# Kernel tuning notes

Hardware: AMD Instinct MI355X
Metric: run time of the kernel (lower is better)

The kernel has to match this reference:

```python
import jax, jax.numpy as jnp
import numpy as np

THRESHOLD = 1000.0  # `threshold` is undefined in the original source; fixed hyperparameter here.


def setup_inputs() -> dict:
    key = jax.random.key(0)
    k1, k2 = jax.random.split(key)
    N, C = 262144, 128
    output = jax.random.normal(k1, (N, C), dtype=jnp.float32)
    target = jax.random.randint(k2, (N,), 0, C, dtype=jnp.int64)
    return {"output": output, "target": target}


def reference(output, target):
    n, c = output.shape
    tgt = target.astype(jnp.int32)
    # score at the target class, per row
    tgt_scores = jnp.take_along_axis(output, tgt[:, None], axis=1)[:, 0]
    # max over the non-target classes (target entry masked to -inf)
    is_tgt = jnp.arange(c)[None, :] == tgt[:, None]
    others_max = jnp.max(jnp.where(is_tgt, -jnp.inf, output), axis=1)
    margin = tgt_scores - others_max
    # soft hinge loss per example
    fst = jax.nn.relu(1.0 - margin)
    snd = jax.nn.relu(1.0 - tgt_scores + jax.scipy.special.logsumexp(output, axis=1))
    l = jnp.where(margin >= 0, fst, snd)
    # partial_opt: sort, cumulative-sum threshold selection, scatter mask back
    order = jnp.argsort(l)
    sorted_l = l[order]
    cum = jnp.cumsum(sorted_l)
    sel = (cum <= THRESHOLD - jnp.arange(n, dtype=l.dtype)).astype(l.dtype)
    v = jnp.zeros((n,), l.dtype).at[order].set(sel)
    curriculum_loss_1 = jnp.dot(v, l)
    curriculum_loss_2 = jnp.asarray(n, l.dtype) - jnp.sum(v)
    return jnp.where(curriculum_loss_1 < curriculum_loss_2, curriculum_loss_2, curriculum_loss_1)
```

## Files before the change

### kernel.cpp

```cpp
#include <hip/hip_runtime.h>
#include <math.h>
#include <stdint.h>


static constexpr int   NBINS     = 128;
static constexpr int   GRID1     = 256;
static constexpr int   BLK1     = 1024;
static constexpr int   CNT_SHIFT = 44;
static constexpr unsigned long long SUM_MASK = (1ULL << CNT_SHIFT) - 1;
static constexpr float BIN_SCALE = 8.0f;
static constexpr float FIX_SCALE = 1048576.0f;
static constexpr double FIX_INV  = 1.0 / 1048576.0;

__device__ __forceinline__ float row_loss(float4 p0, float4 p1, int t, int lane)
{
    const int sl = lane & 15;
    const float v0 = p0.x, v1 = p0.y, v2 = p0.z, v3 = p0.w;
    const float v4 = p1.x, v5 = p1.y, v6 = p1.z, v7 = p1.w;
    const int c0 = sl * 4;
    const int c1 = 64 + sl * 4;

    float mall = fmaxf(fmaxf(fmaxf(v0, v1), fmaxf(v2, v3)),
                       fmaxf(fmaxf(v4, v5), fmaxf(v6, v7)));

    float e0 = (c0 + 0 == t) ? -INFINITY : v0;
    float e1 = (c0 + 1 == t) ? -INFINITY : v1;
    float e2 = (c0 + 2 == t) ? -INFINITY : v2;
    float e3 = (c0 + 3 == t) ? -INFINITY : v3;
    float e4 = (c1 + 0 == t) ? -INFINITY : v4;
    float e5 = (c1 + 1 == t) ? -INFINITY : v5;
    float e6 = (c1 + 2 == t) ? -INFINITY : v6;
    float e7 = (c1 + 3 == t) ? -INFINITY : v7;
    float mexc = fmaxf(fmaxf(fmaxf(e0, e1), fmaxf(e2, e3)),
                       fmaxf(fmaxf(e4, e5), fmaxf(e6, e7)));

    #pragma unroll
    for (int off = 8; off; off >>= 1) {
        mall = fmaxf(mall, __shfl_xor(mall, off));
        mexc = fmaxf(mexc, __shfl_xor(mexc, off));
    }

    float se = __expf(v0 - mall) + __expf(v1 - mall)
             + __expf(v2 - mall) + __expf(v3 - mall)
             + __expf(v4 - mall) + __expf(v5 - mall)
             + __expf(v6 - mall) + __expf(v7 - mall);
    #pragma unroll
    for (int off = 8; off; off >>= 1) se += __shfl_xor(se, off);

    const int te = t & 3;
    const float lo = (te == 0) ? v0 : (te == 1) ? v1 : (te == 2) ? v2 : v3;
    const float hi = (te == 0) ? v4 : (te == 1) ? v5 : (te == 2) ? v6 : v7;
    const float tsv = (t < 64) ? lo : hi;
    const float ts  = __shfl(tsv, (lane & 48) | ((t >> 2) & 15));

    const float margin = ts - mexc;
    const float lse    = mall + __logf(se);
    const float fst    = fmaxf(1.0f - margin, 0.0f);
    const float snd    = fmaxf(1.0f - ts + lse, 0.0f);
    return (margin >= 0.0f) ? fst : snd;
}

__device__ __forceinline__ unsigned long long pack_l(float l)
{
    const int bin = min((int)(l * BIN_SCALE), NBINS - 1);
    const unsigned long long fx =
        (unsigned long long)fminf(l * FIX_SCALE, 16777215.0f);
    return ((unsigned long long)bin << 56) | (1ULL << CNT_SHIFT) | fx;
}

__global__ __launch_bounds__(1024) void closs_fused(
    const float* __restrict__ outm, const int* __restrict__ tgt,
    unsigned long long* __restrict__ parts, int nrows)
{
    __shared__ unsigned long long h[NBINS];
    if (threadIdx.x < NBINS) h[threadIdx.x] = 0ULL;
    __syncthreads();

    const int lane = threadIdx.x & 63;
    const int g    = lane >> 4;
    const int sl   = lane & 15;
    const int wid  = (int)((blockIdx.x * BLK1 + threadIdx.x) >> 6);
    const int nw   = (GRID1 * BLK1) >> 6;

    const float4 z = make_float4(0.f, 0.f, 0.f, 0.f);
    for (int base = wid * 8; base < nrows; base += nw * 8) {
        const int  rA = base + g,   rB = base + 4 + g;
        const bool aA = rA < nrows, aB = rB < nrows;

        float4 a0 = z, a1 = z, b0 = z, b1 = z;
        int ta = 0, tb = 0;
        if (aA) {
            const float4* rp = reinterpret_cast<const float4*>(outm + (size_t)rA * 128);
            a0 = rp[sl]; a1 = rp[sl + 16]; ta = tgt[rA];
        }
        if (aB) {
            const float4* rp = reinterpret_cast<const float4*>(outm + (size_t)rB * 128);
            b0 = rp[sl]; b1 = rp[sl + 16]; tb = tgt[rB];
        }
        const float lA = row_loss(a0, a1, ta, lane);
        const float lB = row_loss(b0, b1, tb, lane);

        if (sl == 0 && aA) {
            const unsigned long long p = pack_l(lA);
            atomicAdd(&h[(int)(p >> 56)], p & 0x00FFFFFFFFFFFFFFULL);
        }
        if (sl == 1 && aB) {
            const unsigned long long p = pack_l(lB);
            atomicAdd(&h[(int)(p >> 56)], p & 0x00FFFFFFFFFFFFFFULL);
        }
    }
    __syncthreads();

    if (threadIdx.x < NBINS)
        parts[(size_t)blockIdx.x * NBINS + threadIdx.x] = h[threadIdx.x];
}

__global__ __launch_bounds__(1024) void closs_final(
    const unsigned long long* __restrict__ parts, unsigned int* __restrict__ outw,
    int nrows)
{
    __shared__ unsigned long long psum[8][NBINS];
    __shared__ unsigned int sc[NBINS];
    __shared__ double       ss[NBINS];
    const int t   = threadIdx.x;
    const int bin = t & (NBINS - 1);
    const int s   = t >> 7;

    unsigned long long acc = 0ULL;
    #pragma unroll 4
    for (int k = 0; k < GRID1 / 8; ++k)
        acc += parts[(size_t)(s * (GRID1 / 8) + k) * NBINS + bin];
    psum[s][bin] = acc;
    __syncthreads();

    unsigned int n = 0; double bs = 0.0;
    if (t < NBINS) {
        unsigned long long v = 0ULL;
        #pragma unroll
        for (int s2 = 0; s2 < 8; ++s2) v += psum[s2][t];
        n  = (unsigned int)(v >> CNT_SHIFT);
        bs = (double)(v & SUM_MASK);
        sc[t] = n; ss[t] = bs;
    }
    __syncthreads();

    for (int off = 1; off < NBINS; off <<= 1) {
        unsigned int cc = 0; double sv = 0.0;
        if (t < NBINS && t >= off) { cc = sc[t - off]; sv = ss[t - off]; }
        __syncthreads();
        if (t < NBINS) { sc[t] += cc; ss[t] += sv; }
        __syncthreads();
    }

    if (t < NBINS) {
        const unsigned int kc = sc[t] - n;
        const double       sf = ss[t] - bs;
        const double S     = sf * FIX_INV;
        const double gfull = S + bs * FIX_INV + (double)kc + (double)n - 1.0;
        const bool crossed_before = (kc > 0) && (S + (double)kc - 1.0 > 1000.0);

        if (n > 0 && gfull > 1000.0 && !crossed_before) {
            const double rem = 1001.0 - (double)kc - S;
            const double av  = bs * FIX_INV / (double)n;
            double j = (rem <= 0.0) ? 0.0 : floor(rem / (av + 1.0));
            if (j > (double)n) j = (double)n;
            if (j < 0.0) j = 0.0;
            const double K   = (double)kc + j;
            const double cl1 = S + j * av;
            const float  A   = fmaxf((float)cl1, (float)((double)nrows - K));
            const unsigned int bits = __float_as_uint(A);
            const unsigned int bf   = (bits + 0x7FFFu + ((bits >> 16) & 1u)) >> 16;
            outw[0] = (bf << 16) | bf;
        }

        if (t == NBINS - 1) {
            const double gall = ss[t] * FIX_INV + (double)sc[t] - 1.0;
            if (sc[t] == 0u || gall <= 1000.0) {
                const float A = fmaxf((float)(ss[t] * FIX_INV),
                                      (float)((double)nrows - (double)sc[t]));
                const unsigned int bits = __float_as_uint(A);
                const unsigned int bf   = (bits + 0x7FFFu + ((bits >> 16) & 1u)) >> 16;
                outw[0] = (bf << 16) | bf;
            }
        }
    }
}

extern "C" void kernel_launch(void* const* d_in, const int* in_sizes, int n_in,
                              void* d_out, int out_size, void* d_ws, size_t ws_size,
                              hipStream_t stream)
{
    const float* outm  = (const float*)d_in[0];
    const int*   tgt   = (const int*)d_in[1];
    const int    nrows = in_sizes[1];

    unsigned long long* parts = (unsigned long long*)d_ws;

    closs_fused<<<GRID1, BLK1, 0, stream>>>(outm, tgt, parts, nrows);
    closs_final<<<1, 1024, 0, stream>>>(parts, (unsigned int*)d_out, nrows);
}
```

Before: 34.08 us.

## Fuse histogram finalize into main kernel via last-block ticket and skip excluded max

Merges the separate finalize kernel into the main histogram kernel. The last block to finish, identified by an atomic ticket counter, performs the scan and threshold selection, which removes one kernel launch and its gap. It also computes the non-target max only when the target score equals the row max, and otherwise reuses the full max. This drops per-element masking and a shuffle reduction for most rows, at the cost of a divergent branch and a threadfence plus global atomic per block.

New measurement: 93.82 us. 175% more time.

```diff
diff --git a/kernel.cpp b/kernel.cpp
--- a/kernel.cpp
+++ b/kernel.cpp
@@ -5,7 +5,7 @@
 
 static constexpr int   NBINS     = 128;
 static constexpr int   GRID1     = 256;
-static constexpr int   BLK1     = 1024;
+static constexpr int   BLK1      = 1024;
 static constexpr int   CNT_SHIFT = 44;
 static constexpr unsigned long long SUM_MASK = (1ULL << CNT_SHIFT) - 1;
 static constexpr float BIN_SCALE = 8.0f;
@@ -17,27 +17,38 @@
     const int sl = lane & 15;
     const float v0 = p0.x, v1 = p0.y, v2 = p0.z, v3 = p0.w;
     const float v4 = p1.x, v5 = p1.y, v6 = p1.z, v7 = p1.w;
-    const int c0 = sl * 4;
-    const int c1 = 64 + sl * 4;
 
     float mall = fmaxf(fmaxf(fmaxf(v0, v1), fmaxf(v2, v3)),
                        fmaxf(fmaxf(v4, v5), fmaxf(v6, v7)));
-
-    float e0 = (c0 + 0 == t) ? -INFINITY : v0;
-    float e1 = (c0 + 1 == t) ? -INFINITY : v1;
-    float e2 = (c0 + 2 == t) ? -INFINITY : v2;
-    float e3 = (c0 + 3 == t) ? -INFINITY : v3;
-    float e4 = (c1 + 0 == t) ? -INFINITY : v4;
-    float e5 = (c1 + 1 == t) ? -INFINITY : v5;
-    float e6 = (c1 + 2 == t) ? -INFINITY : v6;
-    float e7 = (c1 + 3 == t) ? -INFINITY : v7;
-    float mexc = fmaxf(fmaxf(fmaxf(e0, e1), fmaxf(e2, e3)),
-                       fmaxf(fmaxf(e4, e5), fmaxf(e6, e7)));
-
     #pragma unroll
-    for (int off = 8; off; off >>= 1) {
+    for (int off = 8; off; off >>= 1)
         mall = fmaxf(mall, __shfl_xor(mall, off));
-        mexc = fmaxf(mexc, __shfl_xor(mexc, off));
+
+    const int te = t & 3;
+    const float lo = (te == 0) ? v0 : (te == 1) ? v1 : (te == 2) ? v2 : v3;
+    const float hi = (te == 0) ? v4 : (te == 1) ? v5 : (te == 2) ? v6 : v7;
+    const float tsv = (t < 64) ? lo : hi;
+    const float ts  = __shfl(tsv, (lane & 48) | ((t >> 2) & 15));
+
+    float mexc;
+    if (ts == mall) {
+        const int c0 = sl * 4, c1 = 64 + sl * 4;
+        float e0 = (c0 + 0 == t) ? -INFINITY : v0;
+        float e1 = (c0 + 1 == t) ? -INFINITY : v1;
+        float e2 = (c0 + 2 == t) ? -INFINITY : v2;
+        float e3 = (c0 + 3 == t) ? -INFINITY : v3;
+        float e4 = (c1 + 0 == t) ? -INFINITY : v4;
+        float e5 = (c1 + 1 == t) ? -INFINITY : v5;
+        float e6 = (c1 + 2 == t) ? -INFINITY : v6;
+        float e7 = (c1 + 3 == t) ? -INFINITY : v7;
+        float m = fmaxf(fmaxf(fmaxf(e0, e1), fmaxf(e2, e3)),
+                        fmaxf(fmaxf(e4, e5), fmaxf(e6, e7)));
+        #pragma unroll
+        for (int off = 8; off; off >>= 1)
+            m = fmaxf(m, __shfl_xor(m, off));
+        mexc = m;
+    } else {
+        mexc = mall;
     }
 
     float se = __expf(v0 - mall) + __expf(v1 - mall)
@@ -47,12 +58,6 @@
     #pragma unroll
     for (int off = 8; off; off >>= 1) se += __shfl_xor(se, off);
 
-    const int te = t & 3;
-    const float lo = (te == 0) ? v0 : (te == 1) ? v1 : (te == 2) ? v2 : v3;
-    const float hi = (te == 0) ? v4 : (te == 1) ? v5 : (te == 2) ? v6 : v7;
-    const float tsv = (t < 64) ? lo : hi;
-    const float ts  = __shfl(tsv, (lane & 48) | ((t >> 2) & 15));
-
     const float margin = ts - mexc;
     const float lse    = mall + __logf(se);
     const float fst    = fmaxf(1.0f - margin, 0.0f);
@@ -68,11 +73,20 @@
     return ((unsigned long long)bin << 56) | (1ULL << CNT_SHIFT) | fx;
 }
 
-__global__ __launch_bounds__(1024) void closs_fused(
+__global__ __launch_bounds__(1024) void closs_all(
     const float* __restrict__ outm, const int* __restrict__ tgt,
-    unsigned long long* __restrict__ parts, int nrows)
-{
+    unsigned long long* __restrict__ parts, unsigned int* __restrict__ ticket,
+    unsigned int* __restrict__ outw, int nrows)
+{
+    __shared__ unsigned int  c0_sh;
+    __shared__ int           win_sh;
     __shared__ unsigned long long h[NBINS];
+    __shared__ unsigned long long psum[8][NBINS];
+    __shared__ unsigned int  sc[NBINS];
+    __shared__ double        ss[NBINS];
+
+    if (threadIdx.x == 0) c0_sh = *(volatile unsigned int*)ticket;
+
     if (threadIdx.x < NBINS) h[threadIdx.x] = 0ULL;
     __syncthreads();
 
@@ -113,15 +127,16 @@
 
     if (threadIdx.x < NBINS)
         parts[(size_t)blockIdx.x * NBINS + threadIdx.x] = h[threadIdx.x];
-}
-
-__global__ __launch_bounds__(1024) void closs_final(
-    const unsigned long long* __restrict__ parts, unsigned int* __restrict__ outw,
-    int nrows)
-{
-    __shared__ unsigned long long psum[8][NBINS];
-    __shared__ unsigned int sc[NBINS];
-    __shared__ double       ss[NBINS];
+    __threadfence();
+
+    if (threadIdx.x == 0) {
+        const unsigned int v = atomicAdd(ticket, 1u);
+        win_sh = (v == c0_sh + (unsigned int)(GRID1 - 1)) ? 1 : 0;
+    }
+    __syncthreads();
+    if (!win_sh) return;
+    __threadfence();
+
     const int t   = threadIdx.x;
     const int bin = t & (NBINS - 1);
     const int s   = t >> 7;
@@ -194,8 +209,10 @@
     const int*   tgt   = (const int*)d_in[1];
     const int    nrows = in_sizes[1];
 
-    unsigned long long* parts = (unsigned long long*)d_ws;
-
-    closs_fused<<<GRID1, BLK1, 0, stream>>>(outm, tgt, parts, nrows);
-    closs_final<<<1, 1024, 0, stream>>>(parts, (unsigned int*)d_out, nrows);
-}
+    unsigned long long* parts  = (unsigned long long*)d_ws;
+    unsigned int*       ticket = (unsigned int*)((char*)d_ws +
+                                 (size_t)GRID1 * NBINS * sizeof(unsigned long long));
+
+    closs_all<<<GRID1, BLK1, 0, stream>>>(outm, tgt, parts, ticket,
+                                          (unsigned int*)d_out, nrows);
+}
```
